# Kernel tuning notes

Measured on AMD Instinct MI355X. Metric: run time of the kernel, lower is better.

Reference implementation:

```python
import jax, jax.numpy as jnp
import numpy as np

B, IN, U = 4096, 256, 128
G, LW, LB = 1000, 64, 32


def setup_inputs() -> dict:
    key = jax.random.key(0)
    ks = jax.random.split(key, 9)
    return {
        "x": jax.random.normal(ks[0], (B, IN), dtype=jnp.float32),
        "eps_w": jax.random.normal(ks[1], (B, LW), dtype=jnp.float32),
        "eps_b": jax.random.normal(ks[2], (B, LB), dtype=jnp.float32),
        "zw_mu": jax.random.normal(ks[3], (G, LW), dtype=jnp.float32) * 0.05,
        "zw_sigma": jax.random.normal(ks[4], (G, LW), dtype=jnp.float32),
        "Wf": jax.random.normal(ks[5], (LW, IN * U), dtype=jnp.float32) * (1.0 / np.sqrt(LW)),
        "zb_mu": jnp.zeros((G, LB), dtype=jnp.float32),
        "zb_sigma": jax.random.normal(ks[6], (G, LB), dtype=jnp.float32),
        "Bf": jax.random.normal(ks[7], (LB, U), dtype=jnp.float32) * (1.0 / np.sqrt(LB)),
        "gid": jax.random.randint(ks[8], (B,), 0, G, dtype=jnp.int32),
    }


def reference(x, eps_w, eps_b, zw_mu, zw_sigma, Wf, zb_mu, zb_sigma, Bf, gid):
    # --- multilevel weights: gather group posterior, reparameterized sample ---
    mu_w = zw_mu[gid]                                  # [B, LW]
    sig_w = jax.nn.softplus(zw_sigma[gid])             # [B, LW]
    zw_samp = mu_w + sig_w * eps_w                     # [B, LW]
    w = (zw_samp @ Wf).reshape(B, IN, U)               # factor out to per-example weights
    # --- multilevel bias ---
    mu_b = zb_mu[gid]                                  # [B, LB]
    sig_b = jax.nn.softplus(zb_sigma[gid])             # [B, LB]
    b = (mu_b + sig_b * eps_b) @ Bf                    # [B, U]
    # --- batched per-example matmul: w^T @ x  (tf.matmul(w, x, transpose_a=True)) ---
    out = jnp.einsum("bi,biu->bu", x, w) + b           # [B, U]
    return out  # activation is None (linear)
```

## Files before the change

kernel.cpp:

```cpp
#include <hip/hip_runtime.h>
#include <hip/hip_bf16.h>
#include <stdint.h>

#define B_SZ   4096
#define IN_SZ  256
#define U_SZ   128
#define G_SZ   1000
#define LW_SZ  64
#define LB_SZ  32
#define K_SZ   (LW_SZ * IN_SZ)

#define BM     128
#define BK     64
#define KSPL   16
#define NSTEP  16
#define NTILE  (K_SZ / BK)
#define CHUNK  (BK * U_SZ)

typedef __attribute__((ext_vector_type(8))) short  bf16x8;
typedef __attribute__((ext_vector_type(4))) float  f32x4;
typedef __attribute__((ext_vector_type(8))) _Float16 f16x8;
typedef __attribute__((ext_vector_type(2))) _Float16 f16x2;
typedef __attribute__((ext_vector_type(4))) _Float16 f16x4;

typedef const void __attribute__((address_space(1)))* gas_ptr;
typedef void __attribute__((address_space(3)))* las_ptr;

__device__ __forceinline__ ushort f2bf(float f) {
    unsigned u = __float_as_uint(f);
    u += 0x7fffu + ((u >> 16) & 1u);
    return (ushort)(u >> 16);
}

__device__ __forceinline__ float softplus_f(float v) {
    return fmaxf(v, 0.0f) + log1pf(__expf(-fabsf(v)));
}

__global__ __launch_bounds__(256) void fmd_prep(
    const float* __restrict__ Wf, const float* __restrict__ x,
    short* __restrict__ wfT, short* __restrict__ xh)
{
    const int tid = threadIdx.x;
    if (blockIdx.x < NTILE) {
        const int t = blockIdx.x;
        __shared__ float lds[64 * 132];
        #pragma unroll
        for (int it = 0; it < 8; ++it) {
            int idx = it * 256 + tid;
            int kk = idx >> 5, u4 = idx & 31;
            float4 v = *reinterpret_cast<const float4*>(&Wf[(t * 64 + kk) * U_SZ + u4 * 4]);
            *reinterpret_cast<float4*>(&lds[kk * 132 + u4 * 4]) = v;
        }
        __syncthreads();
        short* chunk = wfT + t * CHUNK;
        #pragma unroll
        for (int g = 0; g < 4; ++g) {
            int p = g * 2048 + tid * 8;
            int u = p >> 6;
            int cc = p & 63;
            int kk0 = cc ^ ((u & 7) << 3);
            union { _Float16 h[8]; f16x8 v; } pk;
            #pragma unroll
            for (int j = 0; j < 8; ++j)
                pk.h[j] = (_Float16)lds[(kk0 + j) * 132 + u];
            *reinterpret_cast<f16x8*>(&chunk[p]) = pk.v;
        }
    } else {
        const int bb = blockIdx.x - NTILE;
        const int mt = bb >> 2, c = bb & 3;
        short* chunk = xh + bb * CHUNK;
        #pragma unroll
        for (int g = 0; g < 4; ++g) {
            int p = g * 2048 + tid * 8;
            int r = p >> 6;
            int cc0 = (p & 63) ^ ((r & 7) << 3);
            const float* src = &x[(mt * BM + r) * IN_SZ + c * 64 + cc0];
            float4 a = *reinterpret_cast<const float4*>(src);
            float4 b = *reinterpret_cast<const float4*>(src + 4);
            union { _Float16 h[8]; f16x8 v; } pk;
            pk.h[0] = (_Float16)a.x; pk.h[1] = (_Float16)a.y;
            pk.h[2] = (_Float16)a.z; pk.h[3] = (_Float16)a.w;
            pk.h[4] = (_Float16)b.x; pk.h[5] = (_Float16)b.y;
            pk.h[6] = (_Float16)b.z; pk.h[7] = (_Float16)b.w;
            *reinterpret_cast<f16x8*>(&chunk[p]) = pk.v;
        }
    }
}

__global__ __launch_bounds__(256, 2) void fmd_gemm4(
    const short* __restrict__ xh,
    const short* __restrict__ wfT,
    const float* __restrict__ zw_mu,
    const float* __restrict__ zw_sigma,
    const float* __restrict__ eps_w,
    const int*   __restrict__ gid,
    _Float16*    __restrict__ part)
{
    const int tid  = threadIdx.x;
    const int lane = tid & 63;
    const int wid  = tid >> 6;
    const int wr   = wid >> 1;
    const int wc   = wid & 1;
    const int bid  = blockIdx.x;
    const int ks   = bid & (KSPL - 1);
    const int mt   = bid >> 4;
    const int m0   = mt * BM;

    __shared__ short As[2][CHUNK];
    __shared__ short Bs[3][CHUNK];

    f16x2 zwp[4][4];
    #pragma unroll
    for (int m = 0; m < 4; ++m) {
        int row = wr * 64 + m * 16 + (lane & 15);
        int b   = m0 + row;
        int g   = gid[b];
        float4 mu = *reinterpret_cast<const float4*>(&zw_mu[g * LW_SZ + ks * 4]);
        float4 sg = *reinterpret_cast<const float4*>(&zw_sigma[g * LW_SZ + ks * 4]);
        float4 ep = *reinterpret_cast<const float4*>(&eps_w[b * LW_SZ + ks * 4]);
        float v0 = mu.x + softplus_f(sg.x) * ep.x;
        float v1 = mu.y + softplus_f(sg.y) * ep.y;
        float v2 = mu.z + softplus_f(sg.z) * ep.z;
        float v3 = mu.w + softplus_f(sg.w) * ep.w;
        _Float16 h0 = (_Float16)v0, h1 = (_Float16)v1, h2 = (_Float16)v2, h3 = (_Float16)v3;
        zwp[m][0] = (f16x2){h0, h0};
        zwp[m][1] = (f16x2){h1, h1};
        zwp[m][2] = (f16x2){h2, h2};
        zwp[m][3] = (f16x2){h3, h3};
    }

    const int soff = wid * 2048 + lane * 8;
    const int doff = wid * 2048;

    {
        const short* sB0 = wfT + (ks * 16 + 0) * CHUNK;
        const short* sA0 = xh + (mt * 4 + 0) * CHUNK;
        const short* sB1 = wfT + (ks * 16 + 4) * CHUNK;
        #pragma unroll
        for (int j = 0; j < 4; ++j)
            __builtin_amdgcn_global_load_lds((gas_ptr)(sB0 + soff + j * 512),
                                             (las_ptr)(&Bs[0][doff + j * 512]), 16, 0, 0);
        #pragma unroll
        for (int j = 0; j < 4; ++j)
            __builtin_amdgcn_global_load_lds((gas_ptr)(sA0 + soff + j * 512),
                                             (las_ptr)(&As[0][doff + j * 512]), 16, 0, 0);
        #pragma unroll
        for (int j = 0; j < 4; ++j)
            __builtin_amdgcn_global_load_lds((gas_ptr)(sB1 + soff + j * 512),
                                             (las_ptr)(&Bs[1][doff + j * 512]), 16, 0, 0);
    }
    asm volatile("s_waitcnt vmcnt(4)" ::: "memory");
    __builtin_amdgcn_s_barrier();

    f32x4 acc[4][4];
    #pragma unroll
    for (int m = 0; m < 4; ++m)
        #pragma unroll
        for (int n = 0; n < 4; ++n)
            acc[m][n] = (f32x4){0.f, 0.f, 0.f, 0.f};

    #pragma unroll
    for (int s = 0; s < NSTEP; ++s) {
        const int c  = s >> 2;
        const int li = s & 3;

        if (s + 2 < NSTEP) {
            const int s2 = s + 2;
            const short* sB = wfT + (ks * 16 + (s2 & 3) * 4 + (s2 >> 2)) * CHUNK;
            short* dB = &Bs[s2 % 3][doff];
            #pragma unroll
            for (int j = 0; j < 4; ++j)
                __builtin_amdgcn_global_load_lds((gas_ptr)(sB + soff + j * 512),
                                                 (las_ptr)(dB + j * 512), 16, 0, 0);
        }
        if (li == 2 && c < 3) {
            const short* sA = xh + (mt * 4 + c + 1) * CHUNK;
            short* dA = &As[(c + 1) & 1][doff];
            #pragma unroll
            for (int j = 0; j < 4; ++j)
                __builtin_amdgcn_global_load_lds((gas_ptr)(sA + soff + j * 512),
                                                 (las_ptr)(dA + j * 512), 16, 0, 0);
        }
        __builtin_amdgcn_sched_barrier(0);

        const short* Ab = As[c & 1];
        const short* Bb = Bs[s % 3];
        __builtin_amdgcn_s_setprio(1);
        #pragma unroll
        for (int kb = 0; kb < 2; ++kb) {
            union { f16x8 v8; f16x2 v2[4]; } af[4], bfv[4], as_[4];
            #pragma unroll
            for (int m = 0; m < 4; ++m) {
                int row = wr * 64 + m * 16 + (lane & 15);
                int si = (row * BK + kb * 32 + (lane >> 4) * 8) ^ ((row & 7) << 3);
                af[m].v8 = *reinterpret_cast<const f16x8*>(&Ab[si]);
            }
            #pragma unroll
            for (int n = 0; n < 4; ++n) {
                int rowu = wc * 64 + n * 16 + (lane & 15);
                int si = (rowu * BK + kb * 32 + (lane >> 4) * 8) ^ ((rowu & 7) << 3);
                bfv[n].v8 = *reinterpret_cast<const f16x8*>(&Bb[si]);
            }
            #pragma unroll
            for (int m = 0; m < 4; ++m) {
                #pragma unroll
                for (int w = 0; w < 4; ++w)
                    as_[m].v2[w] = af[m].v2[w] * zwp[m][li];
            }
            #pragma unroll
            for (int m = 0; m < 4; ++m)
                #pragma unroll
                for (int n = 0; n < 4; ++n)
                    acc[m][n] = __builtin_amdgcn_mfma_f32_16x16x32_f16(
                        as_[m].v8, bfv[n].v8, acc[m][n], 0, 0, 0);
        }
        __builtin_amdgcn_s_setprio(0);

        if (s == 14) {
            asm volatile("s_waitcnt vmcnt(0) lgkmcnt(0)" ::: "memory");
            __builtin_amdgcn_s_barrier();
        } else if (s == 15) {
        } else if (li == 2) {
            asm volatile("s_waitcnt vmcnt(8) lgkmcnt(0)" ::: "memory");
            __builtin_amdgcn_s_barrier();
        } else {
            asm volatile("s_waitcnt vmcnt(4) lgkmcnt(0)" ::: "memory");
            __builtin_amdgcn_s_barrier();
        }
    }

    _Float16* dst = part + (size_t)ks * (B_SZ * U_SZ);
    #pragma unroll
    for (int m = 0; m < 4; ++m) {
        int row0 = m0 + wr * 64 + m * 16 + ((lane >> 4) << 2);
        #pragma unroll
        for (int n = 0; n < 4; ++n) {
            int col = wc * 64 + n * 16 + (lane & 15);
            #pragma unroll
            for (int j = 0; j < 4; ++j)
                dst[(row0 + j) * U_SZ + col] = (_Float16)acc[m][n][j];
        }
    }
}

__global__ __launch_bounds__(256) void fmd_reduce2(
    const _Float16* __restrict__ part,
    const float* __restrict__ eps_b,
    const float* __restrict__ zb_mu,
    const float* __restrict__ zb_sigma,
    const float* __restrict__ Bf,
    const int*   __restrict__ gid,
    float*       __restrict__ out)
{
    const int tid = threadIdx.x;
    const int bid = blockIdx.x;
    const int i   = bid * 256 + tid;
    const int bl  = tid >> 5;
    const int u4  = tid & 31;

    __shared__ float zb[8][33];
    {
        int b2 = bid * 8 + bl;
        int g  = gid[b2];
        float sg = softplus_f(zb_sigma[g * LB_SZ + u4]);
        zb[bl][u4] = zb_mu[g * LB_SZ + u4] + sg * eps_b[b2 * LB_SZ + u4];
    }
    __syncthreads();

    const f32x4* Bf4 = (const f32x4*)Bf;
    f32x4 acc = (f32x4){0.f, 0.f, 0.f, 0.f};
    #pragma unroll
    for (int l = 0; l < LB_SZ; ++l)
        acc += zb[bl][l] * Bf4[l * 32 + u4];

    #pragma unroll
    for (int ks = 0; ks < KSPL; ++ks) {
        f16x4 p = *reinterpret_cast<const f16x4*>(&part[(size_t)ks * (B_SZ * U_SZ) + (size_t)i * 4]);
        acc[0] += (float)p[0];
        acc[1] += (float)p[1];
        acc[2] += (float)p[2];
        acc[3] += (float)p[3];
    }
    ((f32x4*)out)[i] = acc;
}

__global__ __launch_bounds__(256) void fmd_bias(
    const float* __restrict__ eps_b,
    const float* __restrict__ zb_mu,
    const float* __restrict__ zb_sigma,
    const float* __restrict__ Bf,
    const int*   __restrict__ gid,
    float*       __restrict__ out)
{
    const int half = threadIdx.x >> 7;
    const int u    = threadIdx.x & 127;
    const int b    = blockIdx.x * 2 + half;

    __shared__ float zb[2][LB_SZ];
    if (u < LB_SZ) {
        int g = gid[b];
        float sg = softplus_f(zb_sigma[g * LB_SZ + u]);
        zb[half][u] = zb_mu[g * LB_SZ + u] + sg * eps_b[b * LB_SZ + u];
    }
    __syncthreads();

    float acc = 0.0f;
    #pragma unroll
    for (int l = 0; l < LB_SZ; ++l)
        acc += zb[half][l] * Bf[l * U_SZ + u];
    out[b * U_SZ + u] = acc;
}

__global__ __launch_bounds__(256, 2) void fmd_gemm_legacy(
    const float* __restrict__ x,
    const float* __restrict__ eps_w,
    const float* __restrict__ zw_mu,
    const float* __restrict__ zw_sigma,
    const float* __restrict__ Wf,
    const int*   __restrict__ gid,
    float*       __restrict__ out)
{
    const int tid  = threadIdx.x;
    const int lane = tid & 63;
    const int wid  = tid >> 6;
    const int wr   = wid >> 1;
    const int wc   = wid & 1;
    const int bid  = blockIdx.x;
    const int ks   = bid & (KSPL - 1);
    const int mt   = bid >> 4;
    const int m0   = mt * BM;

    __shared__ short As[BM * BK];
    __shared__ short Bs[U_SZ * BK];
    __shared__ float zw_s[BM][4];

    for (int it = tid; it < BM * 4; it += 256) {
        int r = it >> 2, lloc = it & 3;
        int b = m0 + r;
        int g = gid[b];
        int l = ks * 4 + lloc;
        float sg = softplus_f(zw_sigma[g * LW_SZ + l]);
        zw_s[r][lloc] = zw_mu[g * LW_SZ + l] + sg * eps_w[b * LW_SZ + l];
    }

    f32x4 acc[4][4];
    #pragma unroll
    for (int m = 0; m < 4; ++m)
        #pragma unroll
        for (int n = 0; n < 4; ++n)
            acc[m][n] = (f32x4){0.f, 0.f, 0.f, 0.f};

    for (int s = 0; s < NSTEP; ++s) {
        __syncthreads();
        const int li = s >> 2;
        const int i0 = (s & 3) * BK;
        const int k0 = ks * (K_SZ / KSPL) + s * BK;

        #pragma unroll
        for (int it = 0; it < 8; ++it) {
            int idx = it * 256 + tid;
            int r = idx >> 4, c4 = idx & 15;
            float4 xv = *reinterpret_cast<const float4*>(&x[(m0 + r) * IN_SZ + i0 + c4 * 4]);
            float zw = zw_s[r][li];
            ushort h0 = f2bf(xv.x * zw), h1 = f2bf(xv.y * zw);
            ushort h2 = f2bf(xv.z * zw), h3 = f2bf(xv.w * zw);
            unsigned long long pw = (unsigned long long)h0
                                  | ((unsigned long long)h1 << 16)
                                  | ((unsigned long long)h2 << 32)
                                  | ((unsigned long long)h3 << 48);
            int si = (r * BK + c4 * 4) ^ ((r & 7) << 3);
            *reinterpret_cast<unsigned long long*>(&As[si]) = pw;
        }
        #pragma unroll
        for (int it = 0; it < 4; ++it) {
            int idx = it * 256 + tid;
            int u = idx & 127, kg = idx >> 7;
            union { ushort h[8]; bf16x8 v; } pk;
            #pragma unroll
            for (int j = 0; j < 8; ++j)
                pk.h[j] = f2bf(Wf[(k0 + kg * 8 + j) * U_SZ + u]);
            int si = (u * BK + kg * 8) ^ ((u & 7) << 3);
            *reinterpret_cast<bf16x8*>(&Bs[si]) = pk.v;
        }
        __syncthreads();

        #pragma unroll
        for (int kb = 0; kb < 2; ++kb) {
            bf16x8 af[4], bfr[4];
            #pragma unroll
            for (int m = 0; m < 4; ++m) {
                int row = wr * 64 + m * 16 + (lane & 15);
                int si = (row * BK + kb * 32 + (lane >> 4) * 8) ^ ((row & 7) << 3);
                af[m] = *reinterpret_cast<const bf16x8*>(&As[si]);
            }
            #pragma unroll
            for (int n = 0; n < 4; ++n) {
                int rowu = wc * 64 + n * 16 + (lane & 15);
                int si = (rowu * BK + kb * 32 + (lane >> 4) * 8) ^ ((rowu & 7) << 3);
                bfr[n] = *reinterpret_cast<const bf16x8*>(&Bs[si]);
            }
            #pragma unroll
            for (int m = 0; m < 4; ++m)
                #pragma unroll
                for (int n = 0; n < 4; ++n)
                    acc[m][n] = __builtin_amdgcn_mfma_f32_16x16x32_bf16(af[m], bfr[n], acc[m][n], 0, 0, 0);
        }
    }

    #pragma unroll
    for (int m = 0; m < 4; ++m) {
        int row0 = m0 + wr * 64 + m * 16 + ((lane >> 4) << 2);
        #pragma unroll
        for (int n = 0; n < 4; ++n) {
            int col = wc * 64 + n * 16 + (lane & 15);
            #pragma unroll
            for (int j = 0; j < 4; ++j)
                atomicAdd(&out[(row0 + j) * U_SZ + col], acc[m][n][j]);
        }
    }
}

extern "C" void kernel_launch(void* const* d_in, const int* in_sizes, int n_in,
                              void* d_out, int out_size, void* d_ws, size_t ws_size,
                              hipStream_t stream) {
    const float* x        = (const float*)d_in[0];
    const float* eps_w    = (const float*)d_in[1];
    const float* eps_b    = (const float*)d_in[2];
    const float* zw_mu    = (const float*)d_in[3];
    const float* zw_sigma = (const float*)d_in[4];
    const float* Wf       = (const float*)d_in[5];
    const float* zb_mu    = (const float*)d_in[6];
    const float* zb_sigma = (const float*)d_in[7];
    const float* Bf       = (const float*)d_in[8];
    const int*   gid      = (const int*)d_in[9];
    float* out = (float*)d_out;

    const size_t WFT_BYTES  = (size_t)K_SZ * U_SZ * 2;
    const size_t XH_OFF     = WFT_BYTES;
    const size_t XH_BYTES   = (size_t)B_SZ * IN_SZ * 2;
    const size_t PART_OFF   = XH_OFF + XH_BYTES;
    const size_t PART_BYTES = (size_t)KSPL * B_SZ * U_SZ * 2;

    if (ws_size >= PART_OFF + PART_BYTES) {
        short*     wfT  = (short*)d_ws;
        short*     xh   = (short*)((char*)d_ws + XH_OFF);
        _Float16*  part = (_Float16*)((char*)d_ws + PART_OFF);
        fmd_prep<<<NTILE + (B_SZ / BM) * 4, 256, 0, stream>>>(Wf, x, wfT, xh);
        fmd_gemm4<<<(B_SZ / BM) * KSPL, 256, 0, stream>>>(
            xh, wfT, zw_mu, zw_sigma, eps_w, gid, part);
        fmd_reduce2<<<(B_SZ * U_SZ) / 1024, 256, 0, stream>>>(
            part, eps_b, zb_mu, zb_sigma, Bf, gid, out);
    } else {
        fmd_bias<<<B_SZ / 2, 256, 0, stream>>>(eps_b, zb_mu, zb_sigma, Bf, gid, out);
        fmd_gemm_legacy<<<(B_SZ / BM) * KSPL, 256, 0, stream>>>(
            x, eps_w, zw_mu, zw_sigma, Wf, gid, out);
    }
}
```

Before: 44.55 us.

## Hold A fragments in registers per chunk, single A buffer, wider reduce

New measurement: 48.84 us. 9.6% more time.

```diff
diff --git a/kernel.cpp b/kernel.cpp
--- a/kernel.cpp
+++ b/kernel.cpp
@@ -43,13 +43,13 @@
     const int tid = threadIdx.x;
     if (blockIdx.x < NTILE) {
         const int t = blockIdx.x;
-        __shared__ float lds[64 * 132];
+        __shared__ float lds[64 * 133];
         #pragma unroll
         for (int it = 0; it < 8; ++it) {
             int idx = it * 256 + tid;
             int kk = idx >> 5, u4 = idx & 31;
             float4 v = *reinterpret_cast<const float4*>(&Wf[(t * 64 + kk) * U_SZ + u4 * 4]);
-            *reinterpret_cast<float4*>(&lds[kk * 132 + u4 * 4]) = v;
+            *reinterpret_cast<float4*>(&lds[kk * 133 + u4 * 4]) = v;
         }
         __syncthreads();
         short* chunk = wfT + t * CHUNK;
@@ -62,7 +62,7 @@
             union { _Float16 h[8]; f16x8 v; } pk;
             #pragma unroll
             for (int j = 0; j < 8; ++j)
-                pk.h[j] = (_Float16)lds[(kk0 + j) * 132 + u];
+                pk.h[j] = (_Float16)lds[(kk0 + j) * 133 + u];
             *reinterpret_cast<f16x8*>(&chunk[p]) = pk.v;
         }
     } else {
@@ -87,7 +87,7 @@
     }
 }
 
-__global__ __launch_bounds__(256, 2) void fmd_gemm4(
+__global__ __launch_bounds__(256, 2) void fmd_gemm5(
     const short* __restrict__ xh,
     const short* __restrict__ wfT,
     const float* __restrict__ zw_mu,
@@ -106,7 +106,7 @@
     const int mt   = bid >> 4;
     const int m0   = mt * BM;
 
-    __shared__ short As[2][CHUNK];
+    __shared__ short As[CHUNK];
     __shared__ short Bs[3][CHUNK];
 
     f16x2 zwp[4][4];
@@ -143,7 +143,7 @@
         #pragma unroll
         for (int j = 0; j < 4; ++j)
             __builtin_amdgcn_global_load_lds((gas_ptr)(sA0 + soff + j * 512),
-                                             (las_ptr)(&As[0][doff + j * 512]), 16, 0, 0);
+                                             (las_ptr)(&As[doff + j * 512]), 16, 0, 0);
         #pragma unroll
         for (int j = 0; j < 4; ++j)
             __builtin_amdgcn_global_load_lds((gas_ptr)(sB1 + soff + j * 512),
@@ -159,73 +159,85 @@
         for (int n = 0; n < 4; ++n)
             acc[m][n] = (f32x4){0.f, 0.f, 0.f, 0.f};
 
-    #pragma unroll
-    for (int s = 0; s < NSTEP; ++s) {
-        const int c  = s >> 2;
-        const int li = s & 3;
-
-        if (s + 2 < NSTEP) {
-            const int s2 = s + 2;
-            const short* sB = wfT + (ks * 16 + (s2 & 3) * 4 + (s2 >> 2)) * CHUNK;
-            short* dB = &Bs[s2 % 3][doff];
-            #pragma unroll
-            for (int j = 0; j < 4; ++j)
-                __builtin_amdgcn_global_load_lds((gas_ptr)(sB + soff + j * 512),
-                                                 (las_ptr)(dB + j * 512), 16, 0, 0);
-        }
-        if (li == 2 && c < 3) {
-            const short* sA = xh + (mt * 4 + c + 1) * CHUNK;
-            short* dA = &As[(c + 1) & 1][doff];
-            #pragma unroll
-            for (int j = 0; j < 4; ++j)
-                __builtin_amdgcn_global_load_lds((gas_ptr)(sA + soff + j * 512),
-                                                 (las_ptr)(dA + j * 512), 16, 0, 0);
-        }
-        __builtin_amdgcn_sched_barrier(0);
-
-        const short* Ab = As[c & 1];
-        const short* Bb = Bs[s % 3];
-        __builtin_amdgcn_s_setprio(1);
-        #pragma unroll
-        for (int kb = 0; kb < 2; ++kb) {
-            union { f16x8 v8; f16x2 v2[4]; } af[4], bfv[4], as_[4];
-            #pragma unroll
-            for (int m = 0; m < 4; ++m) {
-                int row = wr * 64 + m * 16 + (lane & 15);
-                int si = (row * BK + kb * 32 + (lane >> 4) * 8) ^ ((row & 7) << 3);
-                af[m].v8 = *reinterpret_cast<const f16x8*>(&Ab[si]);
-            }
-            #pragma unroll
-            for (int n = 0; n < 4; ++n) {
-                int rowu = wc * 64 + n * 16 + (lane & 15);
-                int si = (rowu * BK + kb * 32 + (lane >> 4) * 8) ^ ((rowu & 7) << 3);
-                bfv[n].v8 = *reinterpret_cast<const f16x8*>(&Bb[si]);
-            }
-            #pragma unroll
-            for (int m = 0; m < 4; ++m) {
-                #pragma unroll
-                for (int w = 0; w < 4; ++w)
-                    as_[m].v2[w] = af[m].v2[w] * zwp[m][li];
-            }
-            #pragma unroll
-            for (int m = 0; m < 4; ++m)
-                #pragma unroll
-                for (int n = 0; n < 4; ++n)
-                    acc[m][n] = __builtin_amdgcn_mfma_f32_16x16x32_f16(
-                        as_[m].v8, bfv[n].v8, acc[m][n], 0, 0, 0);
-        }
-        __builtin_amdgcn_s_setprio(0);
-
-        if (s == 14) {
-            asm volatile("s_waitcnt vmcnt(0) lgkmcnt(0)" ::: "memory");
-            __builtin_amdgcn_s_barrier();
-        } else if (s == 15) {
-        } else if (li == 2) {
-            asm volatile("s_waitcnt vmcnt(8) lgkmcnt(0)" ::: "memory");
-            __builtin_amdgcn_s_barrier();
-        } else {
-            asm volatile("s_waitcnt vmcnt(4) lgkmcnt(0)" ::: "memory");
-            __builtin_amdgcn_s_barrier();
+    for (int c = 0; c < 4; ++c) {
+        union { f16x8 v8; f16x2 v2[4]; } areg[2][4];
+
+        #pragma unroll
+        for (int li = 0; li < 4; ++li) {
+            const int s = c * 4 + li;
+
+            if (s + 2 < NSTEP) {
+                const int s2 = s + 2;
+                const short* sB = wfT + (ks * 16 + (s2 & 3) * 4 + (s2 >> 2)) * CHUNK;
+                short* dB = &Bs[s2 % 3][doff];
+                #pragma unroll
+                for (int j = 0; j < 4; ++j)
+                    __builtin_amdgcn_global_load_lds((gas_ptr)(sB + soff + j * 512),
+                                                     (las_ptr)(dB + j * 512), 16, 0, 0);
+            }
+            if (li == 1 && c < 3) {
+                const short* sA = xh + (mt * 4 + c + 1) * CHUNK;
+                #pragma unroll
+                for (int j = 0; j < 4; ++j)
+                    __builtin_amdgcn_global_load_lds((gas_ptr)(sA + soff + j * 512),
+                                                     (las_ptr)(&As[doff + j * 512]), 16, 0, 0);
+            }
+            __builtin_amdgcn_sched_barrier(0);
+
+            if (li == 0) {
+                #pragma unroll
+                for (int kb = 0; kb < 2; ++kb)
+                    #pragma unroll
+                    for (int m = 0; m < 4; ++m) {
+                        int row = wr * 64 + m * 16 + (lane & 15);
+                        int si = (row * BK + kb * 32 + (lane >> 4) * 8) ^ ((row & 7) << 3);
+                        areg[kb][m].v8 = *reinterpret_cast<const f16x8*>(&As[si]);
+                    }
+            }
+
+            const short* Bb = Bs[s % 3];
+            __builtin_amdgcn_s_setprio(1);
+            #pragma unroll
+            for (int kb = 0; kb < 2; ++kb) {
+                union { f16x8 v8; f16x2 v2[4]; } bfv[4], as_[4];
+                #pragma unroll
+                for (int n = 0; n < 4; ++n) {
+                    int rowu = wc * 64 + n * 16 + (lane & 15);
+                    int si = (rowu * BK + kb * 32 + (lane >> 4) * 8) ^ ((rowu & 7) << 3);
+                    bfv[n].v8 = *reinterpret_cast<const f16x8*>(&Bb[si]);
+                }
+                #pragma unroll
+                for (int m = 0; m < 4; ++m) {
+                    #pragma unroll
+                    for (int w = 0; w < 4; ++w)
+                        as_[m].v2[w] = areg[kb][m].v2[w] * zwp[m][li];
+                }
+                #pragma unroll
+                for (int m = 0; m < 4; ++m)
+                    #pragma unroll
+                    for (int n = 0; n < 4; ++n)
+                        acc[m][n] = __builtin_amdgcn_mfma_f32_16x16x32_f16(
+                            as_[m].v8, bfv[n].v8, acc[m][n], 0, 0, 0);
+            }
+            __builtin_amdgcn_s_setprio(0);
+
+            if (li == 0) {
+                asm volatile("s_waitcnt vmcnt(4) lgkmcnt(0)" ::: "memory");
+                __builtin_amdgcn_s_barrier();
+            } else if (li == 1) {
+                if (c < 3) { asm volatile("s_waitcnt vmcnt(8) lgkmcnt(0)" ::: "memory"); }
+                else       { asm volatile("s_waitcnt vmcnt(4) lgkmcnt(0)" ::: "memory"); }
+                __builtin_amdgcn_s_barrier();
+            } else if (li == 2) {
+                if (c < 3) { asm volatile("s_waitcnt vmcnt(8) lgkmcnt(0)" ::: "memory"); }
+                else       { asm volatile("s_waitcnt vmcnt(0) lgkmcnt(0)" ::: "memory"); }
+                __builtin_amdgcn_s_barrier();
+            } else {
+                if (s != NSTEP - 1) {
+                    asm volatile("s_waitcnt vmcnt(4) lgkmcnt(0)" ::: "memory");
+                    __builtin_amdgcn_s_barrier();
+                }
+            }
         }
     }
 
@@ -238,12 +250,13 @@
             int col = wc * 64 + n * 16 + (lane & 15);
             #pragma unroll
             for (int j = 0; j < 4; ++j)
-                dst[(row0 + j) * U_SZ + col] = (_Float16)acc[m][n][j];
-        }
-    }
-}
-
-__global__ __launch_bounds__(256) void fmd_reduce2(
+                __builtin_nontemporal_store((_Float16)acc[m][n][j],
+                                            &dst[(row0 + j) * U_SZ + col]);
+        }
+    }
+}
+
+__global__ __launch_bounds__(256) void fmd_reduce3(
     const _Float16* __restrict__ part,
     const float* __restrict__ eps_b,
     const float* __restrict__ zb_mu,
@@ -254,34 +267,48 @@
 {
     const int tid = threadIdx.x;
     const int bid = blockIdx.x;
-    const int i   = bid * 256 + tid;
-    const int bl  = tid >> 5;
-    const int u4  = tid & 31;
-
-    __shared__ float zb[8][33];
+    const int i8  = bid * 256 + tid;
+    const int r   = tid >> 4;
+    const int u0  = (tid & 15) * 8;
+
+    __shared__ float zb[16][33];
     {
-        int b2 = bid * 8 + bl;
+        int e = tid;
+        int rr = e >> 5, cc = e & 31;
+        int b2 = bid * 16 + rr;
         int g  = gid[b2];
-        float sg = softplus_f(zb_sigma[g * LB_SZ + u4]);
-        zb[bl][u4] = zb_mu[g * LB_SZ + u4] + sg * eps_b[b2 * LB_SZ + u4];
+        zb[rr][cc] = zb_mu[g * LB_SZ + cc]
+                   + softplus_f(zb_sigma[g * LB_SZ + cc]) * eps_b[b2 * LB_SZ + cc];
+        e += 256; rr = e >> 5; cc = e & 31;
+        b2 = bid * 16 + rr;
+        g  = gid[b2];
+        zb[rr][cc] = zb_mu[g * LB_SZ + cc]
+                   + softplus_f(zb_sigma[g * LB_SZ + cc]) * eps_b[b2 * LB_SZ + cc];
     }
     __syncthreads();
 
-    const f32x4* Bf4 = (const f32x4*)Bf;
-    f32x4 acc = (f32x4){0.f, 0.f, 0.f, 0.f};
-    #pragma unroll
-    for (int l = 0; l < LB_SZ; ++l)
-        acc += zb[bl][l] * Bf4[l * 32 + u4];
+    f32x4 a0 = (f32x4){0.f, 0.f, 0.f, 0.f};
+    f32x4 a1 = (f32x4){0.f, 0.f, 0.f, 0.f};
+    #pragma unroll
+    for (int l = 0; l < LB_SZ; ++l) {
+        float z = zb[r][l];
+        f32x4 b0 = *reinterpret_cast<const f32x4*>(&Bf[l * U_SZ + u0]);
+        f32x4 b1 = *reinterpret_cast<const f32x4*>(&Bf[l * U_SZ + u0 + 4]);
+        a0 += z * b0;
+        a1 += z * b1;
+    }
 
     #pragma unroll
     for (int ks = 0; ks < KSPL; ++ks) {
-        f16x4 p = *reinterpret_cast<const f16x4*>(&part[(size_t)ks * (B_SZ * U_SZ) + (size_t)i * 4]);
-        acc[0] += (float)p[0];
-        acc[1] += (float)p[1];
-        acc[2] += (float)p[2];
-        acc[3] += (float)p[3];
-    }
-    ((f32x4*)out)[i] = acc;
+        f16x8 p = __builtin_nontemporal_load(
+            reinterpret_cast<const f16x8*>(&part[(size_t)ks * (B_SZ * U_SZ) + (size_t)i8 * 8]));
+        a0[0] += (float)p[0]; a0[1] += (float)p[1];
+        a0[2] += (float)p[2]; a0[3] += (float)p[3];
+        a1[0] += (float)p[4]; a1[1] += (float)p[5];
+        a1[2] += (float)p[6]; a1[3] += (float)p[7];
+    }
+    *reinterpret_cast<f32x4*>(&out[(size_t)i8 * 8])     = a0;
+    *reinterpret_cast<f32x4*>(&out[(size_t)i8 * 8 + 4]) = a1;
 }
 
 __global__ __launch_bounds__(256) void fmd_bias(
@@ -446,9 +473,9 @@
         short*     xh   = (short*)((char*)d_ws + XH_OFF);
         _Float16*  part = (_Float16*)((char*)d_ws + PART_OFF);
         fmd_prep<<<NTILE + (B_SZ / BM) * 4, 256, 0, stream>>>(Wf, x, wfT, xh);
-        fmd_gemm4<<<(B_SZ / BM) * KSPL, 256, 0, stream>>>(
+        fmd_gemm5<<<(B_SZ / BM) * KSPL, 256, 0, stream>>>(
             xh, wfT, zw_mu, zw_sigma, eps_w, gid, part);
-        fmd_reduce2<<<(B_SZ * U_SZ) / 1024, 256, 0, stream>>>(
+        fmd_reduce3<<<(B_SZ * U_SZ) / 2048, 256, 0, stream>>>(
             part, eps_b, zb_mu, zb_sigma, Bf, gid, out);
     } else {
         fmd_bias<<<B_SZ / 2, 256, 0, stream>>>(eps_b, zb_mu, zb_sigma, Bf, gid, out);
```
